# Optimization experiments

Hardware: AMD Instinct MI355X
Metric: run time of the kernel (lower is better)

## Reference

```python
import jax, jax.numpy as jnp
import numpy as np

STRIDE, PAD, DIL, DG, K = 1, 1, 1, 1, 3  # conv hyperparams from init_kwargs


def setup_inputs() -> dict:
    key = jax.random.key(0)
    k1, k2, k3, k4, k5 = jax.random.split(key, 5)
    N, C, H, W, Co = 8, 128, 96, 96, 128
    K2 = K * K
    x = jax.random.normal(k1, (N, C, H, W), jnp.float32)
    offset = jax.random.normal(k2, (N, 2 * DG * K2, H, W), jnp.float32)
    mask = jax.random.uniform(k3, (N, DG * K2, H, W), jnp.float32)  # post-sigmoid modulation
    weight = jax.random.normal(k4, (Co, C, K, K), jnp.float32) * 0.05
    bias = jax.random.normal(k5, (Co,), jnp.float32) * 0.05
    return {"x": x, "offset": offset, "mask": mask, "weight": weight, "bias": bias}


def modulated_deform_conv2d(x, offset, mask, weight, bias):
    N, C, H, W = x.shape
    Co = weight.shape[0]
    K2 = K * K
    Ho = (H + 2 * PAD - DIL * (K - 1) - 1) // STRIDE + 1
    Wo = (W + 2 * PAD - DIL * (K - 1) - 1) // STRIDE + 1
    Cg = C // DG

    # offsets: [N, dg, K2, 2(y,x), Ho, Wo]; mask: [N, dg, K2, Ho, Wo]
    off = offset.reshape(N, DG, K2, 2, Ho, Wo)
    m = mask.reshape(N, DG, K2, Ho, Wo)

    ky, kx = jnp.meshgrid(jnp.arange(K), jnp.arange(K), indexing="ij")
    ky = ky.reshape(-1).astype(jnp.float32)  # [K2]
    kx = kx.reshape(-1).astype(jnp.float32)
    base_y = (jnp.arange(Ho, dtype=jnp.float32) * STRIDE - PAD)  # [Ho]
    base_x = (jnp.arange(Wo, dtype=jnp.float32) * STRIDE - PAD)  # [Wo]

    # sampling positions: [N, dg, K2, Ho, Wo]
    py = base_y[None, None, None, :, None] + (ky * DIL)[None, None, :, None, None] + off[:, :, :, 0]
    px = base_x[None, None, None, None, :] + (kx * DIL)[None, None, :, None, None] + off[:, :, :, 1]

    y0 = jnp.floor(py)
    x0 = jnp.floor(px)
    wy = (py - y0).reshape(N, DG, 1, -1)  # frac weights, broadcast over Cg
    wx = (px - x0).reshape(N, DG, 1, -1)
    y0i = y0.astype(jnp.int32)
    x0i = x0.astype(jnp.int32)

    xg = x.reshape(N, DG, Cg, H * W)

    def gather(iy, ix):
        valid = ((iy >= 0) & (iy < H) & (ix >= 0) & (ix < W)).reshape(N, DG, 1, -1)
        idx = (jnp.clip(iy, 0, H - 1) * W + jnp.clip(ix, 0, W - 1)).reshape(N, DG, 1, -1)
        v = jnp.take_along_axis(xg, idx, axis=-1)  # [N, dg, Cg, K2*Ho*Wo]
        return v * valid.astype(x.dtype)

    # bilinear with zero padding outside the image
    v = (gather(y0i, x0i) * (1 - wy) * (1 - wx)
         + gather(y0i, x0i + 1) * (1 - wy) * wx
         + gather(y0i + 1, x0i) * wy * (1 - wx)
         + gather(y0i + 1, x0i + 1) * wy * wx)  # [N, dg, Cg, K2*Ho*Wo]

    v = v.reshape(N, DG, Cg, K2, Ho * Wo) * m.reshape(N, DG, 1, K2, Ho * Wo)
    v = v.reshape(N, C, K2, Ho * Wo)

    out = jnp.einsum("nckp,ock->nop", v, weight.reshape(Co, C, K2))
    out = out + bias[None, :, None]
    return out.reshape(N, Co, Ho, Wo)


def reference(x, offset, mask, weight, bias):
    return modulated_deform_conv2d(x, offset, mask, weight, bias)
```

## Files before the change

kernel.cpp:

```cpp
#include <hip/hip_runtime.h>


#define NI 8
#define CI 128
#define HI 96
#define WI 96
#define CO 128
#define K2 9
#define P_TOT 9216
#define TP 64
#define NTILE 144
#define CPAD 40
#define XT_ELEMS ((size_t)NI * P_TOT * CI)
#define WT_ELEMS ((size_t)K2 * CO * CI)
#define WS_NEED ((XT_ELEMS + WT_ELEMS) * 2)

typedef short short8 __attribute__((ext_vector_type(8)));
typedef float f32x4 __attribute__((ext_vector_type(4)));

static __device__ __forceinline__ ushort bf16_rne(float x) {
    unsigned u = __float_as_uint(x);
    u = (u + 0x7FFF + ((u >> 16) & 1)) >> 16;
    return (ushort)u;
}
static __device__ __forceinline__ unsigned pack_bf2(float a, float b) {
    return (unsigned)bf16_rne(a) | ((unsigned)bf16_rne(b) << 16);
}
static __device__ __forceinline__ unsigned cvt_pk_bf16(float a, float b) {
    unsigned r;
    asm("v_cvt_pk_bf16_f32 %0, %1, %2" : "=v"(r) : "v"(a), "v"(b));
    return r;
}
static __device__ __forceinline__ float bflo(unsigned u) { return __uint_as_float(u << 16); }
static __device__ __forceinline__ float bfhi(unsigned u) { return __uint_as_float(u & 0xFFFF0000u); }

union U4S8 { uint4 u; short8 s; };

static __device__ __forceinline__ void gll16(const ushort* g, ushort* l) {
    __builtin_amdgcn_global_load_lds(
        (const __attribute__((address_space(1))) unsigned int*)g,
        (__attribute__((address_space(3))) unsigned int*)l, 16, 0, 0);
}

__global__ __launch_bounds__(256)
void pre_kernel(const float* __restrict__ x, const float* __restrict__ w,
                ushort* __restrict__ xt, ushort* __restrict__ wt) {
    const int bid = blockIdx.x;
    const int tid = threadIdx.x;
    if (bid < 2304) {
        __shared__ ushort t[64][68];
        const int n = bid / 288, rr = bid % 288;
        const int cblk = rr & 1, hw0 = (rr >> 1) * 64;
        #pragma unroll
        for (int j = 0; j < 4; ++j) {
            int item = j * 256 + tid;
            int c = item >> 4, q = item & 15;
            float4 f = *(const float4*)(x + ((size_t)(n * CI + cblk * 64 + c)) * P_TOT
                                        + hw0 + q * 4);
            t[q * 4 + 0][c] = bf16_rne(f.x);
            t[q * 4 + 1][c] = bf16_rne(f.y);
            t[q * 4 + 2][c] = bf16_rne(f.z);
            t[q * 4 + 3][c] = bf16_rne(f.w);
        }
        __syncthreads();
        #pragma unroll
        for (int j = 0; j < 4; ++j) {
            int item = j * 256 + tid;
            int row = item >> 4, seg = item & 15;
            uint2 v = *(const uint2*)&t[row][seg * 4];
            *(uint2*)(xt + ((size_t)n * P_TOT + hw0 + row) * CI + cblk * 64 + seg * 4) = v;
        }
    } else {
        int s = (bid - 2304) * 256 + tid;
        int k   = s >> 11;
        int r2  = s & 2047;
        int o   = r2 >> 4;
        int csw = r2 & 15;
        int cs  = csw ^ (o & 7);
        const float* src = w + (size_t)o * (CI * K2) + cs * 8 * K2 + k;
        ushort tmp[8];
        #pragma unroll
        for (int j = 0; j < 8; ++j) tmp[j] = bf16_rne(src[j * K2]);
        *(uint4*)&wt[(size_t)s * 8] = *(uint4*)tmp;
    }
}

__global__ __launch_bounds__(256, 2)
void dcn_mfma4_kernel(const ushort* __restrict__ xt,
                      const ushort* __restrict__ wt,
                      const float* __restrict__ offset,
                      const float* __restrict__ mask,
                      const float* __restrict__ bias,
                      float* __restrict__ out)
{
    __shared__ uint2  s_midx[K2 * TP];
    __shared__ float4 s_mw[K2 * TP];
    __shared__ ushort s_w[2][CO * CI];

    const int tid  = threadIdx.x;
    const int bid  = blockIdx.x;
    const int n    = bid & 7;
    const int tile = bid >> 3;
    const int ty   = tile / 6;
    const int tx   = tile - ty * 6;
    const int wave = tid >> 6;
    const int lane = tid & 63;
    const int l15  = lane & 15;
    const int quad = lane >> 4;
    const int gp   = lane >> 2;
    const int gq   = lane & 3;
    const int permaddr = (l15 * 4 + quad) * 4;

    auto stage = [&](int k, int buf) {
        const ushort* g = wt + ((size_t)k * 2048 + wave * 512) * 8;
        ushort* l = &s_w[buf][wave * 512 * 8];
        #pragma unroll
        for (int i = 0; i < 8; ++i)
            gll16(g + (size_t)(i * 64 + lane) * 8, l + i * 64 * 8);
    };

    stage(0, 0);

    for (int itm = 0; itm < 3; ++itm) {
        int item = itm * 256 + tid;
        if (item < K2 * TP) {
            int k = item / TP;
            int i = item % TP;
            int iy = i >> 4, ix = i & 15;
            int ph = ty * 4 + iy;
            int pw = tx * 16 + ix;
            int p  = ph * WI + pw;
            float offy = offset[((size_t)n * (2 * K2) + 2 * k    ) * P_TOT + p];
            float offx = offset[((size_t)n * (2 * K2) + 2 * k + 1) * P_TOT + p];
            float m    = mask  [((size_t)n * K2 + k) * P_TOT + p];
            int ky = k / 3, kx = k % 3;
            float py = (float)(ph - 1 + ky) + offy;
            float px = (float)(pw - 1 + kx) + offx;
            float y0f = floorf(py), x0f = floorf(px);
            float wy = py - y0f, wx = px - x0f;
            int y0 = (int)y0f, x0 = (int)x0f;
            int y1 = y0 + 1,  x1 = x0 + 1;
            bool vy0 = (y0 >= 0) && (y0 < HI);
            bool vy1 = (y1 >= 0) && (y1 < HI);
            bool vx0 = (x0 >= 0) && (x0 < WI);
            bool vx1 = (x1 >= 0) && (x1 < WI);
            unsigned i00 = (vy0 && vx0) ? (unsigned)(y0 * WI + x0) : 0u;
            unsigned i01 = (vy0 && vx1) ? (unsigned)(y0 * WI + x1) : 0u;
            unsigned i10 = (vy1 && vx0) ? (unsigned)(y1 * WI + x0) : 0u;
            unsigned i11 = (vy1 && vx1) ? (unsigned)(y1 * WI + x1) : 0u;
            float w00 = (vy0 && vx0) ? (1.f - wy) * (1.f - wx) * m : 0.f;
            float w01 = (vy0 && vx1) ? (1.f - wy) * wx          * m : 0.f;
            float w10 = (vy1 && vx0) ? wy * (1.f - wx)          * m : 0.f;
            float w11 = (vy1 && vx1) ? wy * wx                  * m : 0.f;
            s_midx[item] = make_uint2(i00 | (i01 << 16), i10 | (i11 << 16));
            s_mw[item]   = make_float4(w00, w01, w10, w11);
        }
    }
    __syncthreads();

    f32x4 acc[8];
    #pragma unroll
    for (int a = 0; a < 8; ++a) acc[a] = (f32x4){0.f, 0.f, 0.f, 0.f};

    const ushort* xbg = xt + (size_t)n * (P_TOT * CI) + gq * 8;
    const int mrow_g = wave * 16 + gp;

    for (int k = 0; k < K2; ++k) {
        const int buf = k & 1;

        uint2  mi = s_midx[k * TP + mrow_g];
        float4 mw = s_mw[k * TP + mrow_g];
        const ushort* c00 = xbg + (size_t)(mi.x & 0xFFFF) * CI;
        const ushort* c01 = xbg + (size_t)(mi.x >> 16)    * CI;
        const ushort* c10 = xbg + (size_t)(mi.y & 0xFFFF) * CI;
        const ushort* c11 = xbg + (size_t)(mi.y >> 16)    * CI;

        uint4 g0[4], g1[4], g2[4], g3[4];
        #pragma unroll
        for (int cb = 0; cb < 4; ++cb) {
            g0[cb] = *(const uint4*)(c00 + cb * 32);
            g1[cb] = *(const uint4*)(c01 + cb * 32);
            g2[cb] = *(const uint4*)(c10 + cb * 32);
            g3[cb] = *(const uint4*)(c11 + cb * 32);
        }

        if (k < 8) stage(k + 1, buf ^ 1);

        #pragma unroll
        for (int cb = 0; cb < 4; ++cb) {
            uint4 r0 = g0[cb], r1 = g1[cb], r2 = g2[cb], r3 = g3[cb];
            float v0 = mw.x * bflo(r0.x) + mw.y * bflo(r1.x) + mw.z * bflo(r2.x) + mw.w * bflo(r3.x);
            float v1 = mw.x * bfhi(r0.x) + mw.y * bfhi(r1.x) + mw.z * bfhi(r2.x) + mw.w * bfhi(r3.x);
            float v2 = mw.x * bflo(r0.y) + mw.y * bflo(r1.y) + mw.z * bflo(r2.y) + mw.w * bflo(r3.y);
            float v3 = mw.x * bfhi(r0.y) + mw.y * bfhi(r1.y) + mw.z * bfhi(r2.y) + mw.w * bfhi(r3.y);
            float v4 = mw.x * bflo(r0.z) + mw.y * bflo(r1.z) + mw.z * bflo(r2.z) + mw.w * bflo(r3.z);
            float v5 = mw.x * bfhi(r0.z) + mw.y * bfhi(r1.z) + mw.z * bfhi(r2.z) + mw.w * bfhi(r3.z);
            float v6 = mw.x * bflo(r0.w) + mw.y * bflo(r1.w) + mw.z * bflo(r2.w) + mw.w * bflo(r3.w);
            float v7 = mw.x * bfhi(r0.w) + mw.y * bfhi(r1.w) + mw.z * bfhi(r2.w) + mw.w * bfhi(r3.w);
            unsigned d0 = cvt_pk_bf16(v0, v1);
            unsigned d1 = cvt_pk_bf16(v2, v3);
            unsigned d2 = cvt_pk_bf16(v4, v5);
            unsigned d3 = cvt_pk_bf16(v6, v7);
            U4S8 cvt;
            cvt.u.x = (unsigned)__builtin_amdgcn_ds_bpermute(permaddr, (int)d0);
            cvt.u.y = (unsigned)__builtin_amdgcn_ds_bpermute(permaddr, (int)d1);
            cvt.u.z = (unsigned)__builtin_amdgcn_ds_bpermute(permaddr, (int)d2);
            cvt.u.w = (unsigned)__builtin_amdgcn_ds_bpermute(permaddr, (int)d3);
            short8 bfr = cvt.s;
            __builtin_amdgcn_s_setprio(1);
            #pragma unroll
            for (int ot = 0; ot < 8; ++ot) {
                int o = ot * 16 + l15;
                short8 afr = *(const short8*)&s_w[buf][o * CI + (((cb * 4 + quad) ^ (o & 7)) * 8)];
                acc[ot] = __builtin_amdgcn_mfma_f32_16x16x32_bf16(afr, bfr, acc[ot], 0, 0, 0);
            }
            __builtin_amdgcn_s_setprio(0);
        }
        __syncthreads();
    }

    const int pbase = (ty * 4 + wave) * WI + tx * 16 + l15;
    #pragma unroll
    for (int ot = 0; ot < 8; ++ot) {
        #pragma unroll
        for (int r = 0; r < 4; ++r) {
            int o = ot * 16 + quad * 4 + r;
            out[((size_t)n * CO + o) * P_TOT + pbase] = acc[ot][r] + bias[o];
        }
    }
}

__global__ __launch_bounds__(256, 3)
void dcn_fallback_kernel(const float* __restrict__ x,
                         const float* __restrict__ offset,
                         const float* __restrict__ mask,
                         const float* __restrict__ weight,
                         const float* __restrict__ bias,
                         float* __restrict__ out)
{
    __shared__ uint2  s_midx[K2 * TP];
    __shared__ float4 s_mw[K2 * TP];
    __shared__ ushort s_v[TP * CPAD];
    __shared__ ushort s_w[CO * CPAD];

    const int tid  = threadIdx.x;
    const int bid  = blockIdx.x;
    const int n    = bid & 7;
    const int p0   = (bid >> 3) * TP;

    for (int it = 0; it < 3; ++it) {
        int item = it * 256 + tid;
        if (item < K2 * TP) {
            int k = item / TP;
            int i = item % TP;
            int p  = p0 + i;
            int ph = p / WI;
            int pw = p % WI;
            float offy = offset[((size_t)n * (2 * K2) + 2 * k    ) * P_TOT + p];
            float offx = offset[((size_t)n * (2 * K2) + 2 * k + 1) * P_TOT + p];
            float m    = mask  [((size_t)n * K2 + k) * P_TOT + p];
            int ky = k / 3, kx = k % 3;
            float py = (float)(ph - 1 + ky) + offy;
            float px = (float)(pw - 1 + kx) + offx;
            float y0f = floorf(py), x0f = floorf(px);
            float wy = py - y0f, wx = px - x0f;
            int y0 = (int)y0f, x0 = (int)x0f;
            int y1 = y0 + 1,  x1 = x0 + 1;
            bool vy0 = (y0 >= 0) && (y0 < HI);
            bool vy1 = (y1 >= 0) && (y1 < HI);
            bool vx0 = (x0 >= 0) && (x0 < WI);
            bool vx1 = (x1 >= 0) && (x1 < WI);
            unsigned i00 = (vy0 && vx0) ? (unsigned)(y0 * WI + x0) : 0u;
            unsigned i01 = (vy0 && vx1) ? (unsigned)(y0 * WI + x1) : 0u;
            unsigned i10 = (vy1 && vx0) ? (unsigned)(y1 * WI + x0) : 0u;
            unsigned i11 = (vy1 && vx1) ? (unsigned)(y1 * WI + x1) : 0u;
            float w00 = (vy0 && vx0) ? (1.f - wy) * (1.f - wx) * m : 0.f;
            float w01 = (vy0 && vx1) ? (1.f - wy) * wx          * m : 0.f;
            float w10 = (vy1 && vx0) ? wy * (1.f - wx)          * m : 0.f;
            float w11 = (vy1 && vx1) ? wy * wx                  * m : 0.f;
            s_midx[item] = make_uint2(i00 | (i01 << 16), i10 | (i11 << 16));
            s_mw[item]   = make_float4(w00, w01, w10, w11);
        }
    }
    __syncthreads();

    const int wave = tid >> 6;
    const int lane = tid & 63;
    const int l15  = lane & 15;
    const int quad = lane >> 4;
    const int o_base = (wave >> 1) * 64;
    const int p_base = (wave & 1) * 32;
    const int gp = tid & 63;
    const int cg = wave;

    f32x4 acc[4][2];
    #pragma unroll
    for (int a = 0; a < 4; ++a)
        #pragma unroll
        for (int b = 0; b < 2; ++b) acc[a][b] = (f32x4){0.f, 0.f, 0.f, 0.f};

    for (int cb = 0; cb < 4; ++cb) {
        for (int k = 0; k < K2; ++k) {
            {
                uint2  mi = s_midx[k * TP + gp];
                float4 mw = s_mw[k * TP + gp];
                int i00 = mi.x & 0xFFFF, i01 = mi.x >> 16;
                int i10 = mi.y & 0xFFFF, i11 = mi.y >> 16;
                const float* xb = x + ((size_t)(n * CI + cb * 32 + cg * 8)) * (HI * WI);
                float v[8];
                #pragma unroll
                for (int j = 0; j < 8; ++j) {
                    const float* xp = xb + (size_t)j * (HI * WI);
                    v[j] = mw.x * xp[i00] + mw.y * xp[i01]
                         + mw.z * xp[i10] + mw.w * xp[i11];
                }
                uint4 pk;
                pk.x = pack_bf2(v[0], v[1]);
                pk.y = pack_bf2(v[2], v[3]);
                pk.z = pack_bf2(v[4], v[5]);
                pk.w = pack_bf2(v[6], v[7]);
                *(uint4*)&s_v[gp * CPAD + cg * 8] = pk;
            }
            {
                int o = tid >> 1, half = tid & 1;
                const float* wsrc = weight + (size_t)o * (CI * K2)
                                  + (cb * 32 + half * 16) * K2 + k;
                ushort tmp[16];
                #pragma unroll
                for (int i = 0; i < 16; ++i) tmp[i] = bf16_rne(wsrc[i * K2]);
                *(uint4*)&s_w[o * CPAD + half * 16]     = *(uint4*)&tmp[0];
                *(uint4*)&s_w[o * CPAD + half * 16 + 8] = *(uint4*)&tmp[8];
            }
            __syncthreads();
            short8 afr[4], bfr[2];
            #pragma unroll
            for (int ot = 0; ot < 4; ++ot)
                afr[ot] = *(const short8*)&s_w[(o_base + ot * 16 + l15) * CPAD + quad * 8];
            #pragma unroll
            for (int pt = 0; pt < 2; ++pt)
                bfr[pt] = *(const short8*)&s_v[(p_base + pt * 16 + l15) * CPAD + quad * 8];
            #pragma unroll
            for (int ot = 0; ot < 4; ++ot)
                #pragma unroll
                for (int pt = 0; pt < 2; ++pt)
                    acc[ot][pt] = __builtin_amdgcn_mfma_f32_16x16x32_bf16(
                        afr[ot], bfr[pt], acc[ot][pt], 0, 0, 0);
            __syncthreads();
        }
    }

    #pragma unroll
    for (int ot = 0; ot < 4; ++ot)
        #pragma unroll
        for (int r = 0; r < 4; ++r) {
            int o = o_base + ot * 16 + quad * 4 + r;
            float b = bias[o];
            #pragma unroll
            for (int pt = 0; pt < 2; ++pt) {
                int p = p0 + p_base + pt * 16 + l15;
                out[((size_t)n * CO + o) * P_TOT + p] = acc[ot][pt][r] + b;
            }
        }
}

extern "C" void kernel_launch(void* const* d_in, const int* in_sizes, int n_in,
                              void* d_out, int out_size, void* d_ws, size_t ws_size,
                              hipStream_t stream) {
    const float* x      = (const float*)d_in[0];
    const float* offset = (const float*)d_in[1];
    const float* mask   = (const float*)d_in[2];
    const float* weight = (const float*)d_in[3];
    const float* bias   = (const float*)d_in[4];
    float* out = (float*)d_out;

    dim3 block(256);
    if (ws_size >= WS_NEED) {
        ushort* xt = (ushort*)d_ws;
        ushort* wt = xt + XT_ELEMS;
        pre_kernel<<<dim3(2304 + 72), block, 0, stream>>>(x, weight, xt, wt);
        dcn_mfma4_kernel<<<dim3(NI * NTILE), block, 0, stream>>>(
            xt, wt, offset, mask, bias, out);
    } else {
        dcn_fallback_kernel<<<dim3(NI * NTILE), block, 0, stream>>>(
            x, offset, mask, weight, bias, out);
    }
}
```

Measured before the change: 168.2 us.

## Software-pipeline bilinear gathers one tap ahead with double-buffered registers

Restructures the 9-tap loop so the global gathers for tap k+1 are issued before the bilinear blend and MFMA work for tap k, using two register sets that alternate. Weight staging for the next tap is moved ahead of the gathers, and the full __syncthreads is replaced by a partial vmcnt wait plus s_barrier. The aim is to hide gather latency behind MFMA compute. The cost is higher register pressure from the extra 16 uint4 registers, which could lower occupancy or cause spills, and the hand-written vmcnt count must match the loads actually in flight.

```diff
diff --git a/kernel.cpp b/kernel.cpp
--- a/kernel.cpp
+++ b/kernel.cpp
@@ -165,17 +165,18 @@
     const ushort* xbg = xt + (size_t)n * (P_TOT * CI) + gq * 8;
     const int mrow_g = wave * 16 + gp;
 
-    for (int k = 0; k < K2; ++k) {
-        const int buf = k & 1;
-
-        uint2  mi = s_midx[k * TP + mrow_g];
-        float4 mw = s_mw[k * TP + mrow_g];
+    uint4 ga0[4], ga1[4], ga2[4], ga3[4];
+    uint4 gb0[4], gb1[4], gb2[4], gb3[4];
+    float4 mwa, mwb;
+
+    auto fetch = [&](int k, uint4 (&g0)[4], uint4 (&g1)[4],
+                     uint4 (&g2)[4], uint4 (&g3)[4], float4& mw) {
+        uint2 mi = s_midx[k * TP + mrow_g];
+        mw = s_mw[k * TP + mrow_g];
         const ushort* c00 = xbg + (size_t)(mi.x & 0xFFFF) * CI;
         const ushort* c01 = xbg + (size_t)(mi.x >> 16)    * CI;
         const ushort* c10 = xbg + (size_t)(mi.y & 0xFFFF) * CI;
         const ushort* c11 = xbg + (size_t)(mi.y >> 16)    * CI;
-
-        uint4 g0[4], g1[4], g2[4], g3[4];
         #pragma unroll
         for (int cb = 0; cb < 4; ++cb) {
             g0[cb] = *(const uint4*)(c00 + cb * 32);
@@ -183,9 +184,10 @@
             g2[cb] = *(const uint4*)(c10 + cb * 32);
             g3[cb] = *(const uint4*)(c11 + cb * 32);
         }
-
-        if (k < 8) stage(k + 1, buf ^ 1);
-
+    };
+
+    auto compute = [&](int buf, uint4 (&g0)[4], uint4 (&g1)[4],
+                       uint4 (&g2)[4], uint4 (&g3)[4], float4 mw) {
         #pragma unroll
         for (int cb = 0; cb < 4; ++cb) {
             uint4 r0 = g0[cb], r1 = g1[cb], r2 = g2[cb], r3 = g3[cb];
@@ -216,8 +218,24 @@
             }
             __builtin_amdgcn_s_setprio(0);
         }
-        __syncthreads();
-    }
+    };
+
+    fetch(0, ga0, ga1, ga2, ga3, mwa);
+
+    for (int kk = 0; kk < 4; ++kk) {
+        const int k = 2 * kk;
+        stage(k + 1, 1);
+        fetch(k + 1, gb0, gb1, gb2, gb3, mwb);
+        compute(0, ga0, ga1, ga2, ga3, mwa);
+        asm volatile("s_waitcnt vmcnt(16)" ::: "memory");
+        __builtin_amdgcn_s_barrier();
+        stage(k + 2, 0);
+        fetch(k + 2, ga0, ga1, ga2, ga3, mwa);
+        compute(1, gb0, gb1, gb2, gb3, mwb);
+        asm volatile("s_waitcnt vmcnt(16)" ::: "memory");
+        __builtin_amdgcn_s_barrier();
+    }
+    compute(0, ga0, ga1, ga2, ga3, mwa);
 
     const int pbase = (ty * 4 + wave) * WI + tx * 16 + l15;
     #pragma unroll
```

After: 165.8 us. Within noise of the previous version (-1.4%).
